# Kernel optimization log

Measured on AMD Instinct MI355X. Metric: run time of the kernel, lower is better.

## Reference

```python
import jax, jax.numpy as jnp
import numpy as np
import math

LMAX = 2
S = (LMAX + 1) ** 2
N_ATOMS = 32000
N_FEAT = 128


def _cg(j1, m1, j2, m2, j3, m3):
    # Clebsch-Gordan coefficient <j1 m1 j2 m2 | j3 m3> via the Racah formula.
    if m3 != m1 + m2 or not (abs(j1 - j2) <= j3 <= j1 + j2):
        return 0.0
    f = math.factorial
    pre = math.sqrt((2 * j3 + 1) * f(j3 + j1 - j2) * f(j3 - j1 + j2) * f(j1 + j2 - j3) / f(j1 + j2 + j3 + 1))
    pre *= math.sqrt(f(j3 + m3) * f(j3 - m3) * f(j1 - m1) * f(j1 + m1) * f(j2 - m2) * f(j2 + m2))
    kmin = max(0, j2 - j3 - m1, j1 - j3 + m2)
    kmax = min(j1 + j2 - j3, j1 - m1, j2 + m2)
    s = 0.0
    for k in range(kmin, kmax + 1):
        s += (-1) ** k / (f(k) * f(j1 + j2 - j3 - k) * f(j1 - m1 - k) * f(j2 + m2 - k) * f(j3 - j2 + m1 + k) * f(j3 - j1 - m2 + k))
    return pre * s


def _build_sparse_cg(lmax):
    # Mirrors schnetpack generate_clebsch_gordan_rsh + nonzero extraction in __init__.
    ls = np.arange(lmax + 1)
    lidx = np.repeat(ls, 2 * ls + 1)
    midx = np.concatenate([np.arange(-l, l + 1) for l in ls])
    n = lidx.shape[0]
    cg = np.zeros((n, n, n))
    for i in range(n):
        for j in range(n):
            for k in range(n):
                cg[i, j, k] = _cg(int(lidx[i]), int(midx[i]), int(lidx[j]), int(midx[j]), int(lidx[k]), int(midx[k]))
    # complex -> real spherical-harmonic unitary change of basis
    U = np.zeros((n, n), dtype=np.complex128)
    off = 0
    for l in ls:
        for m in range(-l, l + 1):
            r = off + l + m
            if m == 0:
                U[r, off + l] = 1.0
            elif m > 0:
                U[r, off + l - m] = 1.0 / np.sqrt(2.0)
                U[r, off + l + m] = (-1.0) ** m / np.sqrt(2.0)
            else:
                am = -m
                U[r, off + l + m] = 1j / np.sqrt(2.0)
                U[r, off + l + am] = -((-1.0) ** am) * 1j / np.sqrt(2.0)
        off += 2 * int(l) + 1
    cg_rsh = np.einsum('ijk,ai,bj,ck->abc', cg.astype(np.complex128), U, U, U.conj())
    parity = (-1.0) ** lidx
    pmask = (parity[:, None, None] * parity[None, :, None]) == parity[None, None, :]
    cg_rsh = np.real(cg_rsh) * pmask
    cg_rsh[np.abs(cg_rsh) < 1e-9] = 0.0
    idx = np.argwhere(cg_rsh != 0.0)
    idx_1, idx_2, idx_out = idx[:, 0], idx[:, 1], idx[:, 2]
    vals = cg_rsh[idx_1, idx_2, idx_out].astype(np.float32)
    return idx_1, idx_2, idx_out, vals, lidx


def setup_inputs() -> dict:
    key = jax.random.key(0)
    k_x, k_w = jax.random.split(key)
    idx_1, idx_2, idx_out, cg_vals, lidx = _build_sparse_cg(LMAX)
    x = jax.random.normal(k_x, (N_ATOMS, S, N_FEAT), dtype=jnp.float32)
    # kaiming_uniform_(a=sqrt(5)) on (lmax+1, lmax+1): bound = 1/sqrt(fan_in)
    bound = 1.0 / math.sqrt(LMAX + 1)
    weight = jax.random.uniform(k_w, (LMAX + 1, LMAX + 1), minval=-bound, maxval=bound, dtype=jnp.float32)
    return {
        "x": x,
        "weight": weight,
        "cg_vals": jnp.asarray(cg_vals),
        "idx_1": jnp.asarray(idx_1, dtype=jnp.int32),
        "idx_2": jnp.asarray(idx_2, dtype=jnp.int32),
        "idx_out": jnp.asarray(idx_out, dtype=jnp.int32),
        "widx_1": jnp.asarray(lidx[idx_1], dtype=jnp.int32),
        "widx_2": jnp.asarray(lidx[idx_2], dtype=jnp.int32),
    }


def reference(x, weight, cg_vals, idx_1, idx_2, idx_out, widx_1, widx_2):
    # y[n, s, f] = sum_{s1,s2} x[n,s1,f] x[n,s2,f] W[l(s1),l(s2)] C[s1,s2,s]
    Wcg = weight[widx_1, widx_2] * cg_vals            # [nnz]
    temp = x[:, idx_1, :] * x[:, idx_2, :] * Wcg[None, :, None]  # [N, nnz, F]
    y = jnp.zeros_like(x).at[:, idx_out, :].add(temp)            # scatter-add over dim 1 -> [N, S, F]
    return y
```

## Files before the change

kernel.cpp:

```cpp
#include <hip/hip_runtime.h>


#define S9 9
#define NFEAT 128
#define THREADS 256
#define NPAIR 45
#define WSTRIDE 12

typedef float f4 __attribute__((ext_vector_type(4)));


__global__ void so3_prep_kernel(const float* __restrict__ weight,
                                const float* __restrict__ cg_vals,
                                const int* __restrict__ idx_1,
                                const int* __restrict__ idx_2,
                                const int* __restrict__ idx_out,
                                const int* __restrict__ widx_1,
                                const int* __restrict__ widx_2,
                                int nnz, float* __restrict__ W) {
    __shared__ float d[NPAIR * WSTRIDE];
    const int tid = threadIdx.x;

    for (int i = tid; i < NPAIR * WSTRIDE; i += THREADS) d[i] = 0.f;
    __syncthreads();

    for (int e = tid; e < nnz; e += THREADS) {
        const int i = idx_1[e];
        const int j = idx_2[e];
        const int k = idx_out[e];
        const float w = weight[widx_1[e] * 3 + widx_2[e]] * cg_vals[e];
        const int a = min(i, j);
        const int b = max(i, j);
        const int p = a * 9 - a * (a - 1) / 2 + (b - a);
        atomicAdd(&d[p * WSTRIDE + k], w);
    }
    __syncthreads();

    for (int i = tid; i < NPAIR * WSTRIDE; i += THREADS) W[i] = d[i];
}

__global__ __launch_bounds__(THREADS) void so3_main_kernel(
        const float* __restrict__ x,
        const float* __restrict__ W,
        float* __restrict__ y) {
    static constexpr int PA[NPAIR] = {
        0,0,0,0,0,0,0,0,0, 1,1,1,1,1,1,1,1, 2,2,2,2,2,2,2,
        3,3,3,3,3,3, 4,4,4,4,4, 5,5,5,5, 6,6,6, 7,7, 8};
    static constexpr int PB[NPAIR] = {
        0,1,2,3,4,5,6,7,8, 1,2,3,4,5,6,7,8, 2,3,4,5,6,7,8,
        3,4,5,6,7,8, 4,5,6,7,8, 5,6,7,8, 6,7,8, 7,8, 8};

    const int gid  = blockIdx.x * THREADS + threadIdx.x;
    const int atom = gid >> 5;
    const int c4   = gid & 31;
    const size_t base = (size_t)atom * (S9 * NFEAT) + (size_t)c4 * 4;

    f4 xv[S9];
    #pragma unroll
    for (int s = 0; s < S9; ++s)
        xv[s] = *(const f4*)(x + base + (size_t)s * NFEAT);

    f4 acc[S9];
    #pragma unroll
    for (int k = 0; k < S9; ++k) acc[k] = (f4)0.f;

    #pragma unroll
    for (int p = 0; p < NPAIR; ++p) {
        const f4 wA = *(const f4*)(W + p * WSTRIDE);
        const f4 wB = *(const f4*)(W + p * WSTRIDE + 4);
        const f4 wC = *(const f4*)(W + p * WSTRIDE + 8);
        const f4 prod = xv[PA[p]] * xv[PB[p]];
        acc[0] = acc[0] + wA[0] * prod;
        acc[1] = acc[1] + wA[1] * prod;
        acc[2] = acc[2] + wA[2] * prod;
        acc[3] = acc[3] + wA[3] * prod;
        acc[4] = acc[4] + wB[0] * prod;
        acc[5] = acc[5] + wB[1] * prod;
        acc[6] = acc[6] + wB[2] * prod;
        acc[7] = acc[7] + wB[3] * prod;
        acc[8] = acc[8] + wC[0] * prod;
    }

    #pragma unroll
    for (int k = 0; k < S9; ++k)
        __builtin_nontemporal_store(acc[k], (f4*)(y + base + (size_t)k * NFEAT));
}

extern "C" void kernel_launch(void* const* d_in, const int* in_sizes, int n_in,
                              void* d_out, int out_size, void* d_ws, size_t ws_size,
                              hipStream_t stream) {
    const float* x       = (const float*)d_in[0];
    const float* weight  = (const float*)d_in[1];
    const float* cg_vals = (const float*)d_in[2];
    const int* idx_1     = (const int*)d_in[3];
    const int* idx_2     = (const int*)d_in[4];
    const int* idx_out   = (const int*)d_in[5];
    const int* widx_1    = (const int*)d_in[6];
    const int* widx_2    = (const int*)d_in[7];
    float* y             = (float*)d_out;
    float* W             = (float*)d_ws;

    const int nnz     = in_sizes[2];
    const int n_atoms = in_sizes[0] / (S9 * NFEAT);

    so3_prep_kernel<<<1, THREADS, 0, stream>>>(weight, cg_vals, idx_1, idx_2,
                                               idx_out, widx_1, widx_2, nnz, W);

    const int total = n_atoms * 32;
    so3_main_kernel<<<total / THREADS, THREADS, 0, stream>>>(x, W, y);
}
```

Before: 65.64 us.

## Process two atom chunks per thread and switch to regular stores

Each thread now handles two f4 feature chunks, one from the first half of the atoms and one from the second half, and issues all loads for both before computing. The goal is more memory-level parallelism per thread and fewer blocks. Nontemporal stores are also replaced with ordinary stores. The cost is higher register pressure from two live sets of x vectors, which may lower occupancy. Correctness relies on the chunk count dividing evenly into 2*THREADS.

Result: slower. 70.15 us (+6.9%).

```diff
diff --git a/kernel.cpp b/kernel.cpp
--- a/kernel.cpp
+++ b/kernel.cpp
@@ -39,31 +39,17 @@
     for (int i = tid; i < NPAIR * WSTRIDE; i += THREADS) W[i] = d[i];
 }
 
-__global__ __launch_bounds__(THREADS) void so3_main_kernel(
-        const float* __restrict__ x,
-        const float* __restrict__ W,
-        float* __restrict__ y) {
+__device__ __forceinline__ void so3_compute(const f4 xv[S9],
+                                            const float* __restrict__ W,
+                                            f4 acc[S9]) {
     static constexpr int PA[NPAIR] = {
         0,0,0,0,0,0,0,0,0, 1,1,1,1,1,1,1,1, 2,2,2,2,2,2,2,
         3,3,3,3,3,3, 4,4,4,4,4, 5,5,5,5, 6,6,6, 7,7, 8};
     static constexpr int PB[NPAIR] = {
         0,1,2,3,4,5,6,7,8, 1,2,3,4,5,6,7,8, 2,3,4,5,6,7,8,
         3,4,5,6,7,8, 4,5,6,7,8, 5,6,7,8, 6,7,8, 7,8, 8};
-
-    const int gid  = blockIdx.x * THREADS + threadIdx.x;
-    const int atom = gid >> 5;
-    const int c4   = gid & 31;
-    const size_t base = (size_t)atom * (S9 * NFEAT) + (size_t)c4 * 4;
-
-    f4 xv[S9];
-    #pragma unroll
-    for (int s = 0; s < S9; ++s)
-        xv[s] = *(const f4*)(x + base + (size_t)s * NFEAT);
-
-    f4 acc[S9];
     #pragma unroll
     for (int k = 0; k < S9; ++k) acc[k] = (f4)0.f;
-
     #pragma unroll
     for (int p = 0; p < NPAIR; ++p) {
         const f4 wA = *(const f4*)(W + p * WSTRIDE);
@@ -80,10 +66,39 @@
         acc[7] = acc[7] + wB[3] * prod;
         acc[8] = acc[8] + wC[0] * prod;
     }
+}
 
+__global__ __launch_bounds__(THREADS) void so3_main_kernel(
+        const float* __restrict__ x,
+        const float* __restrict__ W,
+        float* __restrict__ y,
+        int total_threads) {
+    const int g = blockIdx.x * THREADS + threadIdx.x;
+
+    const int atomA = g >> 5,                 c4A = g & 31;
+    const int gB    = g + total_threads;
+    const int atomB = gB >> 5,                c4B = gB & 31;
+    const size_t baseA = (size_t)atomA * (S9 * NFEAT) + (size_t)c4A * 4;
+    const size_t baseB = (size_t)atomB * (S9 * NFEAT) + (size_t)c4B * 4;
+
+    f4 xvA[S9], xvB[S9];
+    #pragma unroll
+    for (int s = 0; s < S9; ++s)
+        xvA[s] = *(const f4*)(x + baseA + (size_t)s * NFEAT);
+    #pragma unroll
+    for (int s = 0; s < S9; ++s)
+        xvB[s] = *(const f4*)(x + baseB + (size_t)s * NFEAT);
+
+    f4 acc[S9];
+    so3_compute(xvA, W, acc);
     #pragma unroll
     for (int k = 0; k < S9; ++k)
-        __builtin_nontemporal_store(acc[k], (f4*)(y + base + (size_t)k * NFEAT));
+        *(f4*)(y + baseA + (size_t)k * NFEAT) = acc[k];
+
+    so3_compute(xvB, W, acc);
+    #pragma unroll
+    for (int k = 0; k < S9; ++k)
+        *(f4*)(y + baseB + (size_t)k * NFEAT) = acc[k];
 }
 
 extern "C" void kernel_launch(void* const* d_in, const int* in_sizes, int n_in,
@@ -106,6 +121,8 @@
     so3_prep_kernel<<<1, THREADS, 0, stream>>>(weight, cg_vals, idx_1, idx_2,
                                                idx_out, widx_1, widx_2, nnz, W);
 
-    const int total = n_atoms * 32;
-    so3_main_kernel<<<total / THREADS, THREADS, 0, stream>>>(x, W, y);
+    const int total_chunks  = n_atoms * 32;
+    const int total_threads = total_chunks / 2;
+    so3_main_kernel<<<total_threads / THREADS, THREADS, 0, stream>>>(
+        x, W, y, total_threads);
 }
```
